# Kernel tuning notes

Measured on AMD Instinct MI355X. Metric: run time of the kernel, lower is better.

The kernel has to match this reference:

```python
import jax, jax.numpy as jnp
import numpy as np

USER_COUNT = 100000
ITEM_COUNT = 100000
DIM = 64
B = 1024
NPOS = 10
NTOP = 50
CLAMP = 40.0
EPS = 1e-05


def setup_inputs() -> dict:
    key = jax.random.key(0)
    k1, k2, k3, k4, k5 = jax.random.split(key, 5)
    user_emb = jax.random.normal(k1, (USER_COUNT, DIM), dtype=jnp.float32) * 0.01
    item_emb = jax.random.normal(k2, (ITEM_COUNT, DIM), dtype=jnp.float32) * 0.01
    batch_user = jax.random.randint(k3, (B,), 0, USER_COUNT)
    pos_items = jax.random.randint(k4, (B, NPOS), 0, ITEM_COUNT)
    top_items = jax.random.randint(k5, (B, NTOP), 0, ITEM_COUNT)
    batch_user_mask = jnp.zeros((B, ITEM_COUNT), dtype=jnp.float32)
    return {
        "user_emb": user_emb,
        "item_emb": item_emb,
        "batch_user": batch_user,
        "pos_items": pos_items,
        "top_items": top_items,
        "batch_user_mask": batch_user_mask,
        "is_final": 1,
    }


def _overall_loss(mat, pos_items, top_items, mask):
    # tops: scores at pos+top indices, [B, NPOS+NTOP]
    tops = jnp.take_along_axis(mat, jnp.concatenate([pos_items, top_items], -1), axis=1)
    tops_els = (jnp.exp(mat) * (1.0 - mask)).sum(1, keepdims=True)  # [B,1]
    els = tops_els - jnp.exp(jnp.take_along_axis(mat, top_items, axis=1)).sum(1, keepdims=True)
    above = tops.reshape(-1, 1)
    below = jnp.broadcast_to(els, (els.shape[0], tops.shape[1])).reshape(-1, 1) + jnp.exp(above)
    below = jnp.log(jnp.clip(below, EPS))
    return -(above - below).sum()


def _rank_loss(mat, pos_items, top_items, mask):
    S_pos = jnp.take_along_axis(mat, pos_items, axis=1)                       # [B,NPOS]
    S_top = jnp.take_along_axis(mat, top_items[:, : NTOP // 2], axis=1)       # [B,NTOP/2]
    exp_masked_sum = (jnp.exp(mat) * (1.0 - mask)).sum(1, keepdims=True)      # [B,1]
    below2 = exp_masked_sum - jnp.exp(S_top).sum(1, keepdims=True)
    above_pos = S_pos.sum(1, keepdims=True)
    above_top = S_top.sum(1, keepdims=True)
    below_pos = jnp.cumsum(jnp.exp(jnp.flip(S_pos, -1)), axis=1)
    below_top = jnp.cumsum(jnp.exp(jnp.flip(S_top, -1)), axis=1)
    below_pos = jnp.log(jnp.clip(below_pos + below2, EPS)).sum(1, keepdims=True)
    below_top = jnp.log(jnp.clip(below_top + below2, EPS)).sum(1, keepdims=True)
    pos_KD_loss = -(above_pos - below_pos).sum()
    S_top_sub = jnp.take_along_axis(mat, top_items[:, : NTOP // 10], axis=1)  # [B,NTOP/10]
    below2_sub = exp_masked_sum - jnp.exp(S_top_sub).sum(1, keepdims=True)
    above_top_sub = S_top_sub.sum(1, keepdims=True)
    below_top_sub = jnp.cumsum(jnp.exp(jnp.flip(S_top_sub, -1)), axis=1)
    below_top_sub = jnp.log(jnp.clip(below_top_sub + below2_sub, EPS)).sum(1, keepdims=True)
    top_KD_loss = -(above_top - below_top).sum() - (above_top_sub - below_top_sub).sum()
    return pos_KD_loss + top_KD_loss / 2


def reference(user_emb, item_emb, batch_user, pos_items, top_items, batch_user_mask, is_final):
    u = user_emb[batch_user]                                  # [B, DIM]
    mat = jnp.clip(u @ item_emb.T, -CLAMP, CLAMP)             # [B, ITEM_COUNT]
    if is_final:
        return _rank_loss(mat, pos_items, top_items, batch_user_mask)
    return _overall_loss(mat, pos_items, top_items, batch_user_mask)
```

## Files before the change

### kernel.cpp

```cpp
#include <hip/hip_runtime.h>
#include <cstddef>
#include <cstdint>

#define USER_COUNT_C 100000
#define ITEM_COUNT_C 100000
#define DIM_C 64
#define B_C 1024
#define NPOS_C 10
#define NTOP_C 50
#define CLAMP_C 40.0f
#define EPS_C 1e-5f

#define NGROUPS 6250
#define GX 64
#define GY 16

using bf16x8 = __attribute__((ext_vector_type(8))) short;
using f32x4  = __attribute__((ext_vector_type(4))) float;

__global__ void zero_ws_kernel(float* __restrict__ ws) {
    ws[threadIdx.x] = 0.0f;
}

__device__ inline short f2bf(float x) {
    uint32_t b = __float_as_uint(x);
    uint32_t r = (b + 0x7fffu + ((b >> 16) & 1u)) >> 16;
    return (short)r;
}

__device__ inline bf16x8 cvt8(const float* __restrict__ p) {
    float4 v0 = *(const float4*)p;
    float4 v1 = *(const float4*)(p + 4);
    bf16x8 r;
    r[0] = f2bf(v0.x); r[1] = f2bf(v0.y); r[2] = f2bf(v0.z); r[3] = f2bf(v0.w);
    r[4] = f2bf(v1.x); r[5] = f2bf(v1.y); r[6] = f2bf(v1.z); r[7] = f2bf(v1.w);
    return r;
}

__global__ __launch_bounds__(256) void prep_items_kernel(
    const float* __restrict__ item_emb, short* __restrict__ item_bf16) {
    const int t = blockIdx.x * 256 + threadIdx.x;
    const int n16 = t & 15;
    const int q   = (t >> 4) & 3;
    const int h   = (t >> 6) & 1;
    const int g   = t >> 7;
    const int i   = g * 16 + n16;
    bf16x8 v = cvt8(item_emb + (size_t)i * DIM_C + h * 32 + q * 8);
    *(bf16x8*)(item_bf16 + (size_t)g * 1024 + h * 512 + q * 128 + n16 * 8) = v;
}

__global__ __launch_bounds__(256, 4) void expsum_mfma8_kernel(
    const float* __restrict__ user_emb,
    const short* __restrict__ item_bf16,
    const int*   __restrict__ batch_user,
    const float* __restrict__ mask,
    float*       __restrict__ exp_sum)
{
    const int tid  = threadIdx.x;
    const int wave = tid >> 6;
    const int lane = tid & 63;
    const int n16  = lane & 15;
    const int quad = lane >> 4;
    const int uBase = blockIdx.y * 64;

    bf16x8 b0[4], b1[4];
    #pragma unroll
    for (int j = 0; j < 4; ++j) {
        const int uidx = batch_user[uBase + j * 16 + n16];
        const float* us = user_emb + (size_t)uidx * DIM_C + quad * 8;
        b0[j] = cvt8(us);
        b1[j] = cvt8(us + 32);
    }

    const float* mbase = mask + (size_t)(uBase + n16) * ITEM_COUNT_C + quad * 4;
    const short* fbase = item_bf16 + quad * 128 + n16 * 8;

    const int bc0 = (int)(((long)blockIdx.x * NGROUPS) / GX);
    const int bc1 = (int)(((long)(blockIdx.x + 1) * NGROUPS) / GX);
    const int wc0 = bc0 + (int)(((long)(bc1 - bc0) * wave) / 4);
    const int wc1 = bc0 + (int)(((long)(bc1 - bc0) * (wave + 1)) / 4);

    float accE[4] = {0.f, 0.f, 0.f, 0.f};

    auto compute = [&](const bf16x8& f0, const bf16x8& f1, const float4* m) {
        f32x4 acc[4];
        #pragma unroll
        for (int j = 0; j < 4; ++j) {
            acc[j] = (f32x4){0.f, 0.f, 0.f, 0.f};
            acc[j] = __builtin_amdgcn_mfma_f32_16x16x32_bf16(f0, b0[j], acc[j], 0, 0, 0);
            acc[j] = __builtin_amdgcn_mfma_f32_16x16x32_bf16(f1, b1[j], acc[j], 0, 0, 0);
        }
        #pragma unroll
        for (int j = 0; j < 4; ++j) {
            const float* mp = (const float*)&m[j];
            #pragma unroll
            for (int r = 0; r < 4; ++r) {
                const float sc = fminf(fmaxf(acc[j][r], -CLAMP_C), CLAMP_C);
                accE[j] += __expf(sc) * (1.0f - mp[r]);
            }
        }
    };

    int c = wc0;
    for (; c + 2 <= wc1; c += 2) {
        const short* fp = fbase + (size_t)c * 1024;
        const bf16x8 f00 = *(const bf16x8*)fp;
        const bf16x8 f01 = *(const bf16x8*)(fp + 512);
        const bf16x8 f10 = *(const bf16x8*)(fp + 1024);
        const bf16x8 f11 = *(const bf16x8*)(fp + 1536);
        float4 m0[4], m1[4];
        #pragma unroll
        for (int j = 0; j < 4; ++j) {
            const float* mp = mbase + (size_t)j * 16 * ITEM_COUNT_C + (size_t)c * 16;
            m0[j] = *(const float4*)mp;
            m1[j] = *(const float4*)(mp + 16);
        }
        compute(f00, f01, m0);
        compute(f10, f11, m1);
    }
    if (c < wc1) {
        const short* fp = fbase + (size_t)c * 1024;
        const bf16x8 f00 = *(const bf16x8*)fp;
        const bf16x8 f01 = *(const bf16x8*)(fp + 512);
        float4 m0[4];
        #pragma unroll
        for (int j = 0; j < 4; ++j)
            m0[j] = *(const float4*)(mbase + (size_t)j * 16 * ITEM_COUNT_C + (size_t)c * 16);
        compute(f00, f01, m0);
    }

    #pragma unroll
    for (int j = 0; j < 4; ++j) {
        accE[j] += __shfl_xor(accE[j], 16, 64);
        accE[j] += __shfl_xor(accE[j], 32, 64);
    }
    if (quad == 0) {
        #pragma unroll
        for (int j = 0; j < 4; ++j)
            atomicAdd(&exp_sum[uBase + j * 16 + n16], accE[j]);
    }
}

__global__ __launch_bounds__(256) void expsum_fallback_kernel(
    const float* __restrict__ user_emb,
    const float* __restrict__ item_emb,
    const int*   __restrict__ batch_user,
    const float* __restrict__ mask,
    float*       __restrict__ exp_sum)
{
    const int tid  = threadIdx.x;
    const int wave = tid >> 6;
    const int lane = tid & 63;
    const int n16  = lane & 15;
    const int quad = lane >> 4;
    const int rowBase = blockIdx.y * 64 + wave * 16;

    const int uidx = batch_user[rowBase + n16];
    const float* usrc = user_emb + (size_t)uidx * DIM_C + quad * 8;
    const bf16x8 a0 = cvt8(usrc);
    const bf16x8 a1 = cvt8(usrc + 32);

    float accExp[4] = {0.f, 0.f, 0.f, 0.f};

    for (int t = blockIdx.x; t < NGROUPS / 4; t += 64) {
        const int ibase = t * 64;
        bf16x8 b0[4], b1[4];
        #pragma unroll
        for (int s = 0; s < 4; ++s) {
            const int gi = ibase + s * 16 + n16;
            const float* isrc = item_emb + (size_t)gi * DIM_C + quad * 8;
            b0[s] = cvt8(isrc);
            b1[s] = cvt8(isrc + 32);
        }
        f32x4 acc[4];
        #pragma unroll
        for (int s = 0; s < 4; ++s) {
            acc[s] = (f32x4){0.f, 0.f, 0.f, 0.f};
            acc[s] = __builtin_amdgcn_mfma_f32_16x16x32_bf16(a0, b0[s], acc[s], 0, 0, 0);
            acc[s] = __builtin_amdgcn_mfma_f32_16x16x32_bf16(a1, b1[s], acc[s], 0, 0, 0);
        }
        #pragma unroll
        for (int s = 0; s < 4; ++s)
            #pragma unroll
            for (int reg = 0; reg < 4; ++reg) {
                const int row = rowBase + quad * 4 + reg;
                const float sc = fminf(fmaxf(acc[s][reg], -CLAMP_C), CLAMP_C);
                const float w = 1.0f - mask[(size_t)row * ITEM_COUNT_C + ibase + s * 16 + n16];
                accExp[reg] += __expf(sc) * w;
            }
    }
    #pragma unroll
    for (int off = 1; off < 16; off <<= 1)
        #pragma unroll
        for (int reg = 0; reg < 4; ++reg)
            accExp[reg] += __shfl_xor(accExp[reg], off, 64);
    if (n16 == 0)
        #pragma unroll
        for (int reg = 0; reg < 4; ++reg)
            atomicAdd(&exp_sum[rowBase + quad * 4 + reg], accExp[reg]);
}

__global__ void finalize_kernel(
    const float* __restrict__ user_emb,
    const float* __restrict__ item_emb,
    const int*   __restrict__ batch_user,
    const int*   __restrict__ pos_items,
    const int*   __restrict__ top_items,
    const float* __restrict__ exp_sum,
    const int*   __restrict__ is_final,
    float*       __restrict__ row_loss)
{
    __shared__ float ush[DIM_C];
    __shared__ float s_sh[NPOS_C + NTOP_C];
    const int b = blockIdx.x;
    const int tid = threadIdx.x;
    const int uidx = batch_user[b];
    if (tid < 16)
        *(float4*)&ush[tid * 4] = *(const float4*)(user_emb + (size_t)uidx * DIM_C + tid * 4);
    __syncthreads();

    if (tid < NPOS_C + NTOP_C) {
        const int idx = (tid < NPOS_C) ? pos_items[b * NPOS_C + tid]
                                       : top_items[b * NTOP_C + (tid - NPOS_C)];
        const float* iv = item_emb + (size_t)idx * DIM_C;
        float s = 0.f;
        #pragma unroll
        for (int d4 = 0; d4 < 16; ++d4) {
            const float4 a = *(const float4*)(iv + d4 * 4);
            s += a.x * ush[d4 * 4 + 0] + a.y * ush[d4 * 4 + 1]
               + a.z * ush[d4 * 4 + 2] + a.w * ush[d4 * 4 + 3];
        }
        s_sh[tid] = fminf(fmaxf(s, -CLAMP_C), CLAMP_C);
    }
    __syncthreads();

    if (tid == 0) {
        const float E = exp_sum[b];
        float L;
        if (is_final[0] != 0) {
            float sumExpTop = 0.f, above_top = 0.f;
            for (int i = 0; i < NTOP_C / 2; ++i) {
                const float v = s_sh[NPOS_C + i];
                sumExpTop += __expf(v); above_top += v;
            }
            const float below2 = E - sumExpTop;
            float above_pos = 0.f;
            for (int i = 0; i < NPOS_C; ++i) above_pos += s_sh[i];
            float c = 0.f, below_pos = 0.f;
            for (int i = 0; i < NPOS_C; ++i) {
                c += __expf(s_sh[NPOS_C - 1 - i]);
                below_pos += __logf(fmaxf(c + below2, EPS_C));
            }
            float c2 = 0.f, below_top = 0.f;
            for (int i = 0; i < NTOP_C / 2; ++i) {
                c2 += __expf(s_sh[NPOS_C + NTOP_C / 2 - 1 - i]);
                below_top += __logf(fmaxf(c2 + below2, EPS_C));
            }
            const float pos_KD = below_pos - above_pos;
            float sumExpSub = 0.f, above_sub = 0.f;
            for (int i = 0; i < NTOP_C / 10; ++i) {
                const float v = s_sh[NPOS_C + i];
                sumExpSub += __expf(v); above_sub += v;
            }
            const float below2s = E - sumExpSub;
            float c3 = 0.f, below_sub = 0.f;
            for (int i = 0; i < NTOP_C / 10; ++i) {
                c3 += __expf(s_sh[NPOS_C + NTOP_C / 10 - 1 - i]);
                below_sub += __logf(fmaxf(c3 + below2s, EPS_C));
            }
            const float top_KD = (below_top - above_top) + (below_sub - above_sub);
            L = pos_KD + 0.5f * top_KD;
        } else {
            float sumExpTop = 0.f;
            for (int i = 0; i < NTOP_C; ++i) sumExpTop += __expf(s_sh[NPOS_C + i]);
            const float els = E - sumExpTop;
            L = 0.f;
            for (int j = 0; j < NPOS_C + NTOP_C; ++j) {
                const float a = s_sh[j];
                L += __logf(fmaxf(els + __expf(a), EPS_C)) - a;
            }
        }
        row_loss[b] = L;
    }
}

__global__ void reduce_kernel(const float* __restrict__ rl, float* __restrict__ out) {
    __shared__ float part[16];
    const int tid = threadIdx.x;
    float v = rl[tid];
    #pragma unroll
    for (int off = 32; off > 0; off >>= 1) v += __shfl_down(v, off, 64);
    if ((tid & 63) == 0) part[tid >> 6] = v;
    __syncthreads();
    if (tid == 0) {
        float s = 0.f;
        #pragma unroll
        for (int i = 0; i < 16; ++i) s += part[i];
        out[0] = s;
    }
}

extern "C" void kernel_launch(void* const* d_in, const int* in_sizes, int n_in,
                              void* d_out, int out_size, void* d_ws, size_t ws_size,
                              hipStream_t stream) {
    const float* user_emb   = (const float*)d_in[0];
    const float* item_emb   = (const float*)d_in[1];
    const int*   batch_user = (const int*)d_in[2];
    const int*   pos_items  = (const int*)d_in[3];
    const int*   top_items  = (const int*)d_in[4];
    const float* mask       = (const float*)d_in[5];
    const int*   is_final   = (const int*)d_in[6];
    float* out = (float*)d_out;

    float* exp_sum  = (float*)d_ws;
    float* row_loss = exp_sum + B_C;
    short* item_bf16 = (short*)(row_loss + B_C);
    const size_t need = 2 * B_C * sizeof(float)
                      + ((size_t)NGROUPS + 16) * 1024 * sizeof(short);

    hipLaunchKernelGGL(zero_ws_kernel, dim3(1), dim3(B_C), 0, stream, exp_sum);
    if (ws_size >= need) {
        hipLaunchKernelGGL(prep_items_kernel, dim3(NGROUPS * 128 / 256), dim3(256),
                           0, stream, item_emb, item_bf16);
        hipLaunchKernelGGL(expsum_mfma8_kernel, dim3(GX, GY), dim3(256),
                           0, stream, user_emb, item_bf16, batch_user, mask, exp_sum);
    } else {
        hipLaunchKernelGGL(expsum_fallback_kernel, dim3(64, B_C / 64), dim3(256),
                           0, stream, user_emb, item_emb, batch_user, mask, exp_sum);
    }
    hipLaunchKernelGGL(finalize_kernel, dim3(B_C), dim3(64), 0, stream,
                       user_emb, item_emb, batch_user, pos_items, top_items,
                       exp_sum, is_final, row_loss);
    hipLaunchKernelGGL(reduce_kernel, dim3(1), dim3(B_C), 0, stream, row_loss, out);
}
```

Baseline: 602.7 us.

## Split mask handling into a streaming scan with sparse exp corrections

The MFMA exp-sum kernel no longer reads the mask; it sums exp over all items. A separate kernel streams the mask as coalesced float4 loads over the whole buffer. For any nonzero entry it recomputes that score in fp32 and atomically accumulates exp(score)*mask into a per-row correction, which finalize subtracts. Zeroing of the accumulators is folded into the prep kernel. The aim is to replace the strided per-row mask reads interleaved with MFMA work by a purely bandwidth-bound pass. The cost is possible cancellation in the subtraction, and slow scalar dot products if the mask is dense.

```diff
diff --git a/kernel.cpp b/kernel.cpp
--- a/kernel.cpp
+++ b/kernel.cpp
@@ -14,12 +14,14 @@
 #define NGROUPS 6250
 #define GX 64
 #define GY 16
+#define NF4 (B_C * ITEM_COUNT_C / 4)
+#define F4_PER_ROW (ITEM_COUNT_C / 4)
 
 using bf16x8 = __attribute__((ext_vector_type(8))) short;
 using f32x4  = __attribute__((ext_vector_type(4))) float;
 
 __global__ void zero_ws_kernel(float* __restrict__ ws) {
-    ws[threadIdx.x] = 0.0f;
+    ws[blockIdx.x * 1024 + threadIdx.x] = 0.0f;
 }
 
 __device__ inline short f2bf(float x) {
@@ -38,8 +40,10 @@
 }
 
 __global__ __launch_bounds__(256) void prep_items_kernel(
-    const float* __restrict__ item_emb, short* __restrict__ item_bf16) {
+    const float* __restrict__ item_emb, short* __restrict__ item_bf16,
+    float* __restrict__ acc_bufs) {
     const int t = blockIdx.x * 256 + threadIdx.x;
+    if (blockIdx.x < 8) acc_bufs[blockIdx.x * 256 + threadIdx.x] = 0.0f;
     const int n16 = t & 15;
     const int q   = (t >> 4) & 3;
     const int h   = (t >> 6) & 1;
@@ -49,11 +53,10 @@
     *(bf16x8*)(item_bf16 + (size_t)g * 1024 + h * 512 + q * 128 + n16 * 8) = v;
 }
 
-__global__ __launch_bounds__(256, 4) void expsum_mfma8_kernel(
+__global__ __launch_bounds__(256, 4) void expsum_nomask_kernel(
     const float* __restrict__ user_emb,
     const short* __restrict__ item_bf16,
     const int*   __restrict__ batch_user,
-    const float* __restrict__ mask,
     float*       __restrict__ exp_sum)
 {
     const int tid  = threadIdx.x;
@@ -71,8 +74,6 @@
         b0[j] = cvt8(us);
         b1[j] = cvt8(us + 32);
     }
-
-    const float* mbase = mask + (size_t)(uBase + n16) * ITEM_COUNT_C + quad * 4;
     const short* fbase = item_bf16 + quad * 128 + n16 * 8;
 
     const int bc0 = (int)(((long)blockIdx.x * NGROUPS) / GX);
@@ -82,7 +83,10 @@
 
     float accE[4] = {0.f, 0.f, 0.f, 0.f};
 
-    auto compute = [&](const bf16x8& f0, const bf16x8& f1, const float4* m) {
+    for (int c = wc0; c < wc1; ++c) {
+        const short* fp = fbase + (size_t)c * 1024;
+        const bf16x8 f0 = *(const bf16x8*)fp;
+        const bf16x8 f1 = *(const bf16x8*)(fp + 512);
         f32x4 acc[4];
         #pragma unroll
         for (int j = 0; j < 4; ++j) {
@@ -91,42 +95,12 @@
             acc[j] = __builtin_amdgcn_mfma_f32_16x16x32_bf16(f1, b1[j], acc[j], 0, 0, 0);
         }
         #pragma unroll
-        for (int j = 0; j < 4; ++j) {
-            const float* mp = (const float*)&m[j];
+        for (int j = 0; j < 4; ++j)
             #pragma unroll
             for (int r = 0; r < 4; ++r) {
                 const float sc = fminf(fmaxf(acc[j][r], -CLAMP_C), CLAMP_C);
-                accE[j] += __expf(sc) * (1.0f - mp[r]);
-            }
-        }
-    };
-
-    int c = wc0;
-    for (; c + 2 <= wc1; c += 2) {
-        const short* fp = fbase + (size_t)c * 1024;
-        const bf16x8 f00 = *(const bf16x8*)fp;
-        const bf16x8 f01 = *(const bf16x8*)(fp + 512);
-        const bf16x8 f10 = *(const bf16x8*)(fp + 1024);
-        const bf16x8 f11 = *(const bf16x8*)(fp + 1536);
-        float4 m0[4], m1[4];
-        #pragma unroll
-        for (int j = 0; j < 4; ++j) {
-            const float* mp = mbase + (size_t)j * 16 * ITEM_COUNT_C + (size_t)c * 16;
-            m0[j] = *(const float4*)mp;
-            m1[j] = *(const float4*)(mp + 16);
-        }
-        compute(f00, f01, m0);
-        compute(f10, f11, m1);
-    }
-    if (c < wc1) {
-        const short* fp = fbase + (size_t)c * 1024;
-        const bf16x8 f00 = *(const bf16x8*)fp;
-        const bf16x8 f01 = *(const bf16x8*)(fp + 512);
-        float4 m0[4];
-        #pragma unroll
-        for (int j = 0; j < 4; ++j)
-            m0[j] = *(const float4*)(mbase + (size_t)j * 16 * ITEM_COUNT_C + (size_t)c * 16);
-        compute(f00, f01, m0);
+                accE[j] += __expf(sc);
+            }
     }
 
     #pragma unroll
@@ -139,6 +113,48 @@
         for (int j = 0; j < 4; ++j)
             atomicAdd(&exp_sum[uBase + j * 16 + n16], accE[j]);
     }
+}
+
+__global__ __launch_bounds__(256) void mask_scan_kernel(
+    const float* __restrict__ mask,
+    const float* __restrict__ user_emb,
+    const float* __restrict__ item_emb,
+    const int*   __restrict__ batch_user,
+    float*       __restrict__ exp_neg)
+{
+    const float4* m4 = (const float4*)mask;
+    const int T = gridDim.x * 256;
+
+    auto handle = [&](float4 v, int q) {
+        if (v.x != 0.f || v.y != 0.f || v.z != 0.f || v.w != 0.f) {
+            const int b  = q / F4_PER_ROW;
+            const int c4 = q - b * F4_PER_ROW;
+            const float* u = user_emb + (size_t)batch_user[b] * DIM_C;
+            const float* mp = (const float*)&v;
+            #pragma unroll
+            for (int k = 0; k < 4; ++k) {
+                const float m = mp[k];
+                if (m != 0.f) {
+                    const float* iv = item_emb + (size_t)(c4 * 4 + k) * DIM_C;
+                    float s = 0.f;
+                    for (int d = 0; d < DIM_C; ++d) s += u[d] * iv[d];
+                    s = fminf(fmaxf(s, -CLAMP_C), CLAMP_C);
+                    atomicAdd(&exp_neg[b], __expf(s) * m);
+                }
+            }
+        }
+    };
+
+    int q = blockIdx.x * 256 + threadIdx.x;
+    for (; q + 3 * T < NF4; q += 4 * T) {
+        const float4 v0 = m4[q];
+        const float4 v1 = m4[q + T];
+        const float4 v2 = m4[q + 2 * T];
+        const float4 v3 = m4[q + 3 * T];
+        handle(v0, q); handle(v1, q + T);
+        handle(v2, q + 2 * T); handle(v3, q + 3 * T);
+    }
+    for (; q < NF4; q += T) handle(m4[q], q);
 }
 
 __global__ __launch_bounds__(256) void expsum_fallback_kernel(
@@ -207,6 +223,7 @@
     const int*   __restrict__ pos_items,
     const int*   __restrict__ top_items,
     const float* __restrict__ exp_sum,
+    const float* __restrict__ exp_neg,
     const int*   __restrict__ is_final,
     float*       __restrict__ row_loss)
 {
@@ -235,7 +252,7 @@
     __syncthreads();
 
     if (tid == 0) {
-        const float E = exp_sum[b];
+        const float E = exp_sum[b] - exp_neg[b];
         float L;
         if (is_final[0] != 0) {
             float sumExpTop = 0.f, above_top = 0.f;
@@ -313,23 +330,26 @@
     float* out = (float*)d_out;
 
     float* exp_sum  = (float*)d_ws;
-    float* row_loss = exp_sum + B_C;
+    float* exp_neg  = exp_sum + B_C;
+    float* row_loss = exp_neg + B_C;
     short* item_bf16 = (short*)(row_loss + B_C);
-    const size_t need = 2 * B_C * sizeof(float)
+    const size_t need = 3 * B_C * sizeof(float)
                       + ((size_t)NGROUPS + 16) * 1024 * sizeof(short);
 
-    hipLaunchKernelGGL(zero_ws_kernel, dim3(1), dim3(B_C), 0, stream, exp_sum);
     if (ws_size >= need) {
         hipLaunchKernelGGL(prep_items_kernel, dim3(NGROUPS * 128 / 256), dim3(256),
-                           0, stream, item_emb, item_bf16);
-        hipLaunchKernelGGL(expsum_mfma8_kernel, dim3(GX, GY), dim3(256),
-                           0, stream, user_emb, item_bf16, batch_user, mask, exp_sum);
+                           0, stream, item_emb, item_bf16, exp_sum);
+        hipLaunchKernelGGL(expsum_nomask_kernel, dim3(GX, GY), dim3(256),
+                           0, stream, user_emb, item_bf16, batch_user, exp_sum);
+        hipLaunchKernelGGL(mask_scan_kernel, dim3(2048), dim3(256),
+                           0, stream, mask, user_emb, item_emb, batch_user, exp_neg);
     } else {
+        hipLaunchKernelGGL(zero_ws_kernel, dim3(2), dim3(1024), 0, stream, exp_sum);
         hipLaunchKernelGGL(expsum_fallback_kernel, dim3(64, B_C / 64), dim3(256),
                            0, stream, user_emb, item_emb, batch_user, mask, exp_sum);
     }
     hipLaunchKernelGGL(finalize_kernel, dim3(B_C), dim3(64), 0, stream,
                        user_emb, item_emb, batch_user, pos_items, top_items,
-                       exp_sum, is_final, row_loss);
+                       exp_sum, exp_neg, is_final, row_loss);
     hipLaunchKernelGGL(reduce_kernel, dim3(1), dim3(B_C), 0, stream, row_loss, out);
 }
```

New measurement: 624.9 us. 3.7% more time.
